# Kernel tuning notes

Hardware: AMD Instinct MI355X
Metric: run time of the kernel (lower is better)

The kernel has to match this reference:

```python
import jax, jax.numpy as jnp
import numpy as np

N, E = 50000, 1600000
FEAT, HID, HEADS = 256, 64, 2
NEG_SLOPE = 0.2


def gat_conv(x, src, dst, W, att_src, att_dst, bias, heads, out_ch):
    """PyG GATConv (concat=True, self-loops already appended to src/dst)."""
    n = x.shape[0]
    h = (x @ W).reshape(n, heads, out_ch)                      # [N,H,C]
    a_src = jnp.einsum('nhc,hc->nh', h, att_src)               # [N,H]
    a_dst = jnp.einsum('nhc,hc->nh', h, att_dst)               # [N,H]
    alpha = jax.nn.leaky_relu(a_src[src] + a_dst[dst], NEG_SLOPE)  # [E',H]
    # segment softmax over incoming edges of each dst node
    amax = jax.ops.segment_max(alpha, dst, num_segments=n)
    alpha = jnp.exp(alpha - amax[dst])
    denom = jax.ops.segment_sum(alpha, dst, num_segments=n)
    alpha = alpha / (denom[dst] + 1e-16)
    msg = h[src] * alpha[..., None]                            # [E',H,C]
    out = jax.ops.segment_sum(msg, dst, num_segments=n)        # [N,H,C]
    return out.reshape(n, heads * out_ch) + bias


def setup_inputs() -> dict:
    key = jax.random.key(0)
    ks = jax.random.split(key, 10)
    x = jax.random.normal(ks[0], (N, FEAT), dtype=jnp.float32)
    edge_index = jax.random.randint(ks[1], (2, E), 0, N, dtype=jnp.int64)
    s1 = 1.0 / np.sqrt(FEAT)
    s2 = 1.0 / np.sqrt(HID * HEADS)
    sa = 1.0 / np.sqrt(HID)
    return {
        'x': x,
        'edge_index': edge_index,
        'W1': jax.random.uniform(ks[2], (FEAT, HEADS * HID), jnp.float32, -s1, s1),
        'att_src1': jax.random.uniform(ks[3], (HEADS, HID), jnp.float32, -sa, sa),
        'att_dst1': jax.random.uniform(ks[4], (HEADS, HID), jnp.float32, -sa, sa),
        'b1': jnp.zeros((HEADS * HID,), jnp.float32),
        'W2': jax.random.uniform(ks[5], (HEADS * HID, HID), jnp.float32, -s2, s2),
        'att_src2': jax.random.uniform(ks[6], (1, HID), jnp.float32, -sa, sa),
        'att_dst2': jax.random.uniform(ks[7], (1, HID), jnp.float32, -sa, sa),
        'b2': jnp.zeros((HID,), jnp.float32),
    }


def reference(x, edge_index, W1, att_src1, att_dst1, b1, W2, att_src2, att_dst2, b2):
    n = x.shape[0]
    loop = jnp.arange(n, dtype=edge_index.dtype)
    src = jnp.concatenate([edge_index[0], loop])   # add self loops (PyG default)
    dst = jnp.concatenate([edge_index[1], loop])
    h = gat_conv(x, src, dst, W1, att_src1, att_dst1, b1, HEADS, HID)
    h = jax.nn.relu(h)  # dropout is identity in eval mode
    h = gat_conv(h, src, dst, W2, att_src2, att_dst2, b2, 1, HID)
    return jax.nn.log_softmax(h, axis=1)
```

## Files before the change

### kernel.cpp

```cpp
#include <hip/hip_runtime.h>
#include <hip/hip_bf16.h>
#include <math.h>

typedef short bf16x8 __attribute__((ext_vector_type(8)));
typedef float f32x4 __attribute__((ext_vector_type(4)));

#define BSHIFT 7
#define BWIDTH 128
#define PCHUNK 4096


__global__ void zero_buf(int* __restrict__ p, int n) {
    int i = blockIdx.x * blockDim.x + threadIdx.x;
    if (i < n) p[i] = 0;
}

__global__ __launch_bounds__(256) void bucket_hist(const int* __restrict__ ei, int E,
                                                   int* __restrict__ bcnt) {
    __shared__ int h[512];
    int tid = threadIdx.x;
    for (int i = tid; i < 512; i += 256) h[i] = 0;
    __syncthreads();
    int start = blockIdx.x * PCHUNK;
    int cnt = min(PCHUNK, E - start);
    for (int i = tid; i < cnt; i += 256)
        atomicAdd(&h[ei[E + start + i] >> BSHIFT], 1);
    __syncthreads();
    for (int i = tid; i < 512; i += 256)
        if (h[i]) atomicAdd(&bcnt[i], h[i]);
}

__global__ __launch_bounds__(512) void bucket_scan(const int* __restrict__ bcnt,
                                                   int* __restrict__ bbase,
                                                   int* __restrict__ bcur,
                                                   int nbk, int n) {
    __shared__ int s[512];
    int tid = threadIdx.x;
    int nodes = 0;
    if (tid < nbk) nodes = min(BWIDTH, n - (tid << BSHIFT));
    int v = (tid < nbk) ? bcnt[tid] + nodes : 0;
    s[tid] = v;
    __syncthreads();
    #pragma unroll
    for (int o = 1; o < 512; o <<= 1) {
        int t = (tid >= o) ? s[tid - o] : 0;
        __syncthreads();
        s[tid] += t;
        __syncthreads();
    }
    if (tid < nbk) {
        int ex = s[tid] - v;
        bbase[tid] = ex;
        bcur[tid] = ex - (tid << BSHIFT);
    }
    if (tid == nbk) bbase[nbk] = s[tid];
}

__global__ __launch_bounds__(256) void partition_edges(const int* __restrict__ ei, int E,
                                                       int* __restrict__ bcur,
                                                       int2* __restrict__ tmp) {
    __shared__ int2 stage[PCHUNK];
    __shared__ int h[512];
    __shared__ int lbase[512];
    int tid = threadIdx.x;
    int start = blockIdx.x * PCHUNK;
    int cnt = min(PCHUNK, E - start);
    for (int i = tid; i < 512; i += 256) h[i] = 0;
    __syncthreads();
    for (int i = tid; i < cnt; i += 256) {
        int s = ei[start + i];
        int d = ei[E + start + i];
        stage[i] = make_int2(s, d);
        atomicAdd(&h[d >> BSHIFT], 1);
    }
    __syncthreads();
    for (int i = tid; i < 512; i += 256) {
        if (h[i] > 0) lbase[i] = atomicAdd(&bcur[i], h[i]);
        h[i] = 0;
    }
    __syncthreads();
    for (int i = tid; i < cnt; i += 256) {
        int2 e = stage[i];
        int b = e.y >> BSHIFT;
        int r = atomicAdd(&h[b], 1);
        tmp[lbase[b] + r] = e;
    }
}

__global__ __launch_bounds__(256) void bucket_csr(const int* __restrict__ bbase,
                                                  const int2* __restrict__ tmp,
                                                  int* __restrict__ offs,
                                                  int* __restrict__ srcs,
                                                  int n, int nbk) {
    __shared__ int cnt[BWIDTH];
    __shared__ int sa[BWIDTH];
    __shared__ int cur[BWIDTH];
    int b = blockIdx.x;
    int tid = threadIdx.x;
    int node0 = b << BSHIFT;
    int nnodes = min(BWIDTH, n - node0);
    int cb = bbase[b];
    int ce = bbase[b + 1];
    int tb = cb - node0;
    int ecnt = (ce - cb) - nnodes;

    if (tid < BWIDTH) cnt[tid] = (tid < nnodes) ? 1 : 0;
    __syncthreads();
    for (int i = tid; i < ecnt; i += 256)
        atomicAdd(&cnt[tmp[tb + i].y & (BWIDTH - 1)], 1);
    __syncthreads();
    if (tid < BWIDTH) sa[tid] = cnt[tid];
    __syncthreads();
    #pragma unroll
    for (int o = 1; o < BWIDTH; o <<= 1) {
        int v = 0;
        if (tid < BWIDTH) { v = sa[tid]; if (tid >= o) v += sa[tid - o]; }
        __syncthreads();
        if (tid < BWIDTH) sa[tid] = v;
        __syncthreads();
    }
    if (tid < BWIDTH) {
        int ex = sa[tid] - cnt[tid];
        if (tid < nnodes) {
            offs[node0 + tid] = cb + ex;
            srcs[cb + ex] = node0 + tid;
        }
        cur[tid] = ex + (tid < nnodes ? 1 : 0);
    }
    if (b == nbk - 1 && tid == 0) offs[n] = ce;
    __syncthreads();
    for (int i = tid; i < ecnt; i += 256) {
        int2 e = tmp[tb + i];
        int li = e.y & (BWIDTH - 1);
        int r = atomicAdd(&cur[li], 1);
        srcs[cb + r] = e.x;
    }
}

__global__ void transpose_both(const float* __restrict__ W1, const float* __restrict__ W2,
                               __hip_bfloat16* __restrict__ W1t,
                               __hip_bfloat16* __restrict__ W2t) {
    int idx = blockIdx.x * blockDim.x + threadIdx.x;
    const int n1 = 128 * 256;
    if (idx < n1) {
        int nn = idx >> 8, kk = idx & 255;
        W1t[idx] = __float2bfloat16(W1[kk * 128 + nn]);
    } else {
        int j = idx - n1;
        if (j < 64 * 128) {
            int nn = j >> 7, kk = j & 127;
            W2t[j] = __float2bfloat16(W2[kk * 64 + nn]);
        }
    }
}

template <bool A_BF16, int NT, int HEADS>
__global__ __launch_bounds__(256) void gemm_att(
    const void* __restrict__ Av, const __hip_bfloat16* __restrict__ Bt,
    __hip_bfloat16* __restrict__ C,
    const float* __restrict__ atts, const float* __restrict__ attd,
    float* __restrict__ a_s, float* __restrict__ a_d, int M, int K) {
    constexpr int N = NT * 16;
    __shared__ __hip_bfloat16 As[64][40];
    int tid = threadIdx.x;
    int w = tid >> 6, l = tid & 63;
    int q = l >> 4, m16 = l & 15;
    int bm = blockIdx.x * 64;

    int lr = tid >> 2, lseg = tid & 3;
    int arow = bm + lr; if (arow >= M) arow = M - 1;

    f32x4 acc[NT];
    #pragma unroll
    for (int t = 0; t < NT; t++) acc[t] = (f32x4){0.f, 0.f, 0.f, 0.f};

    for (int kc = 0; kc < K; kc += 32) {
        if (A_BF16) {
            const __hip_bfloat16* A = (const __hip_bfloat16*)Av;
            uint4 v = *(const uint4*)(A + (size_t)arow * K + kc + lseg * 8);
            *(uint4*)&As[lr][lseg * 8] = v;
        } else {
            const float* A = (const float*)Av;
            float4 v0 = *(const float4*)(A + (size_t)arow * K + kc + lseg * 8);
            float4 v1 = *(const float4*)(A + (size_t)arow * K + kc + lseg * 8 + 4);
            union { __hip_bfloat16 h[8]; uint4 u; } tmp;
            tmp.h[0] = __float2bfloat16(v0.x); tmp.h[1] = __float2bfloat16(v0.y);
            tmp.h[2] = __float2bfloat16(v0.z); tmp.h[3] = __float2bfloat16(v0.w);
            tmp.h[4] = __float2bfloat16(v1.x); tmp.h[5] = __float2bfloat16(v1.y);
            tmp.h[6] = __float2bfloat16(v1.z); tmp.h[7] = __float2bfloat16(v1.w);
            *(uint4*)&As[lr][lseg * 8] = tmp.u;
        }
        __syncthreads();
        bf16x8 a = *(const bf16x8*)&As[w * 16 + m16][q * 8];
        #pragma unroll
        for (int t = 0; t < NT; t++) {
            bf16x8 b = *(const bf16x8*)(Bt + (size_t)(t * 16 + m16) * K + kc + q * 8);
            acc[t] = __builtin_amdgcn_mfma_f32_16x16x32_bf16(a, b, acc[t], 0, 0, 0);
        }
        __syncthreads();
    }

    #pragma unroll
    for (int t = 0; t < NT; t++) {
        #pragma unroll
        for (int r = 0; r < 4; r++) {
            int row = bm + w * 16 + q * 4 + r;
            if (row < M) C[(size_t)row * N + t * 16 + m16] = __float2bfloat16(acc[t][r]);
        }
    }

    float ps[HEADS][4], pd[HEADS][4];
    #pragma unroll
    for (int hh = 0; hh < HEADS; hh++)
        #pragma unroll
        for (int r = 0; r < 4; r++) { ps[hh][r] = 0.f; pd[hh][r] = 0.f; }
    #pragma unroll
    for (int t = 0; t < NT; t++) {
        int ch = t * 16 + m16;
        float asw = atts[ch], adw = attd[ch];
        int hh = (HEADS == 2) ? (t >> 2) : 0;
        #pragma unroll
        for (int r = 0; r < 4; r++) {
            ps[hh][r] = fmaf(acc[t][r], asw, ps[hh][r]);
            pd[hh][r] = fmaf(acc[t][r], adw, pd[hh][r]);
        }
    }
    #pragma unroll
    for (int o = 1; o < 16; o <<= 1) {
        #pragma unroll
        for (int hh = 0; hh < HEADS; hh++)
            #pragma unroll
            for (int r = 0; r < 4; r++) {
                ps[hh][r] += __shfl_xor(ps[hh][r], o);
                pd[hh][r] += __shfl_xor(pd[hh][r], o);
            }
    }
    if (m16 == 0) {
        #pragma unroll
        for (int r = 0; r < 4; r++) {
            int row = bm + w * 16 + q * 4 + r;
            if (row < M) {
                if (HEADS == 2) {
                    a_s[row * 2]     = ps[0][r];
                    a_s[row * 2 + 1] = ps[1][r];
                    a_d[row * 2]     = pd[0][r];
                    a_d[row * 2 + 1] = pd[1][r];
                } else {
                    a_s[row] = ps[0][r];
                    a_d[row] = pd[0][r];
                }
            }
        }
    }
}

__device__ __forceinline__ float leaky(float r) {
    return r < 0.f ? 0.2f * r : r;
}

__device__ __forceinline__ void unpack2(unsigned u, float& lo, float& hi) {
    lo = __uint_as_float(u << 16);
    hi = __uint_as_float(u & 0xffff0000u);
}

__global__ __launch_bounds__(256) void edge_agg_l1(
    const int* __restrict__ offs, const int* __restrict__ srcs,
    const __hip_bfloat16* __restrict__ h1, const float* __restrict__ asv,
    const float* __restrict__ adv, const float* __restrict__ bias,
    __hip_bfloat16* __restrict__ out, int n) {
    int d = (blockIdx.x * blockDim.x + threadIdx.x) >> 6;
    int lane = threadIdx.x & 63;
    if (d >= n) return;
    int start = offs[d], end = offs[d + 1];
    float ad0 = adv[2 * d], ad1 = adv[2 * d + 1];

    float m0 = -3.4e38f, m1 = -3.4e38f, s0 = 0.f, s1 = 0.f;
    for (int e = start + lane; e < end; e += 64) {
        int s = srcs[e];
        float2 a = *(const float2*)(asv + 2 * s);
        float r0 = leaky(a.x + ad0);
        float r1 = leaky(a.y + ad1);
        if (r0 > m0) { s0 *= __expf(m0 - r0); m0 = r0; }
        s0 += __expf(r0 - m0);
        if (r1 > m1) { s1 *= __expf(m1 - r1); m1 = r1; }
        s1 += __expf(r1 - m1);
    }
    #pragma unroll
    for (int o = 1; o < 64; o <<= 1) {
        float om0 = __shfl_xor(m0, o), os0 = __shfl_xor(s0, o);
        float nm0 = fmaxf(m0, om0);
        s0 = s0 * __expf(m0 - nm0) + os0 * __expf(om0 - nm0);
        m0 = nm0;
        float om1 = __shfl_xor(m1, o), os1 = __shfl_xor(s1, o);
        float nm1 = fmaxf(m1, om1);
        s1 = s1 * __expf(m1 - nm1) + os1 * __expf(om1 - nm1);
        m1 = nm1;
    }
    float inv0 = 1.f / (s0 + 1e-16f), inv1 = 1.f / (s1 + 1e-16f);

    int sub = lane & 15;
    int g = lane >> 4;
    int ch0 = sub * 8;
    int hsel = sub >> 3;

    float acc[8];
    #pragma unroll
    for (int k = 0; k < 8; k++) acc[k] = 0.f;

    for (int base = start; base < end; base += 64) {
        int cnt = min(64, end - base);
        int s_l = 0;
        float w0_l = 0.f, w1_l = 0.f;
        if (lane < cnt) {
            s_l = srcs[base + lane];
            float2 a = *(const float2*)(asv + 2 * s_l);
            w0_l = __expf(leaky(a.x + ad0) - m0) * inv0;
            w1_l = __expf(leaky(a.y + ad1) - m1) * inv1;
        }
        int steps = (cnt + 3) >> 2;
        for (int jj = 0; jj < steps; ++jj) {
            int e = jj * 4 + g;
            float w0e = __shfl(w0_l, e);
            float w1e = __shfl(w1_l, e);
            int se = __shfl(s_l, e);
            float we = hsel ? w1e : w0e;
            uint4 v = *(const uint4*)(h1 + (size_t)se * 128 + ch0);
            float f0, f1, f2, f3, f4, f5, f6, f7;
            unpack2(v.x, f0, f1);
            unpack2(v.y, f2, f3);
            unpack2(v.z, f4, f5);
            unpack2(v.w, f6, f7);
            acc[0] = fmaf(we, f0, acc[0]);
            acc[1] = fmaf(we, f1, acc[1]);
            acc[2] = fmaf(we, f2, acc[2]);
            acc[3] = fmaf(we, f3, acc[3]);
            acc[4] = fmaf(we, f4, acc[4]);
            acc[5] = fmaf(we, f5, acc[5]);
            acc[6] = fmaf(we, f6, acc[6]);
            acc[7] = fmaf(we, f7, acc[7]);
        }
    }
    #pragma unroll
    for (int o = 16; o < 64; o <<= 1)
        #pragma unroll
        for (int k = 0; k < 8; k++) acc[k] += __shfl_xor(acc[k], o);

    if (lane < 16) {
        float4 b0 = *(const float4*)(bias + ch0);
        float4 b1 = *(const float4*)(bias + ch0 + 4);
        union { __hip_bfloat16 h[8]; uint4 u; } o2;
        o2.h[0] = __float2bfloat16(fmaxf(acc[0] + b0.x, 0.f));
        o2.h[1] = __float2bfloat16(fmaxf(acc[1] + b0.y, 0.f));
        o2.h[2] = __float2bfloat16(fmaxf(acc[2] + b0.z, 0.f));
        o2.h[3] = __float2bfloat16(fmaxf(acc[3] + b0.w, 0.f));
        o2.h[4] = __float2bfloat16(fmaxf(acc[4] + b1.x, 0.f));
        o2.h[5] = __float2bfloat16(fmaxf(acc[5] + b1.y, 0.f));
        o2.h[6] = __float2bfloat16(fmaxf(acc[6] + b1.z, 0.f));
        o2.h[7] = __float2bfloat16(fmaxf(acc[7] + b1.w, 0.f));
        *(uint4*)(out + (size_t)d * 128 + ch0) = o2.u;
    }
}

__global__ __launch_bounds__(256) void edge_agg_l2(
    const int* __restrict__ offs, const int* __restrict__ srcs,
    const __hip_bfloat16* __restrict__ h2, const float* __restrict__ asv,
    const float* __restrict__ adv, const float* __restrict__ bias,
    float* __restrict__ out, int n) {
    int d = (blockIdx.x * blockDim.x + threadIdx.x) >> 6;
    int lane = threadIdx.x & 63;
    if (d >= n) return;
    int start = offs[d], end = offs[d + 1];
    float ad = adv[d];

    float m = -3.4e38f, ssum = 0.f;
    for (int e = start + lane; e < end; e += 64) {
        int s = srcs[e];
        float r = leaky(asv[s] + ad);
        if (r > m) { ssum *= __expf(m - r); m = r; }
        ssum += __expf(r - m);
    }
    #pragma unroll
    for (int o = 1; o < 64; o <<= 1) {
        float om = __shfl_xor(m, o), os = __shfl_xor(ssum, o);
        float nm = fmaxf(m, om);
        ssum = ssum * __expf(m - nm) + os * __expf(om - nm);
        m = nm;
    }
    float inv = 1.f / (ssum + 1e-16f);

    int sub = lane & 7;
    int g = lane >> 3;
    int ch0 = sub * 8;

    float acc[8];
    #pragma unroll
    for (int k = 0; k < 8; k++) acc[k] = 0.f;

    for (int base = start; base < end; base += 64) {
        int cnt = min(64, end - base);
        int s_l = 0;
        float w_l = 0.f;
        if (lane < cnt) {
            s_l = srcs[base + lane];
            w_l = __expf(leaky(asv[s_l] + ad) - m) * inv;
        }
        int steps = (cnt + 7) >> 3;
        for (int jj = 0; jj < steps; ++jj) {
            int e = jj * 8 + g;
            float we = __shfl(w_l, e);
            int se = __shfl(s_l, e);
            uint4 v = *(const uint4*)(h2 + (size_t)se * 64 + ch0);
            float f0, f1, f2, f3, f4, f5, f6, f7;
            unpack2(v.x, f0, f1);
            unpack2(v.y, f2, f3);
            unpack2(v.z, f4, f5);
            unpack2(v.w, f6, f7);
            acc[0] = fmaf(we, f0, acc[0]);
            acc[1] = fmaf(we, f1, acc[1]);
            acc[2] = fmaf(we, f2, acc[2]);
            acc[3] = fmaf(we, f3, acc[3]);
            acc[4] = fmaf(we, f4, acc[4]);
            acc[5] = fmaf(we, f5, acc[5]);
            acc[6] = fmaf(we, f6, acc[6]);
            acc[7] = fmaf(we, f7, acc[7]);
        }
    }
    #pragma unroll
    for (int o = 8; o < 64; o <<= 1)
        #pragma unroll
        for (int k = 0; k < 8; k++) acc[k] += __shfl_xor(acc[k], o);

    float4 b0 = *(const float4*)(bias + ch0);
    float4 b1 = *(const float4*)(bias + ch0 + 4);
    float v[8];
    v[0] = acc[0] + b0.x; v[1] = acc[1] + b0.y;
    v[2] = acc[2] + b0.z; v[3] = acc[3] + b0.w;
    v[4] = acc[4] + b1.x; v[5] = acc[5] + b1.y;
    v[6] = acc[6] + b1.z; v[7] = acc[7] + b1.w;

    float vm = v[0];
    #pragma unroll
    for (int k = 1; k < 8; k++) vm = fmaxf(vm, v[k]);
    #pragma unroll
    for (int o = 1; o < 8; o <<= 1) vm = fmaxf(vm, __shfl_xor(vm, o));
    float se_loc = 0.f;
    #pragma unroll
    for (int k = 0; k < 8; k++) se_loc += __expf(v[k] - vm);
    #pragma unroll
    for (int o = 1; o < 8; o <<= 1) se_loc += __shfl_xor(se_loc, o);
    float lse = vm + logf(se_loc);

    if (lane < 8) {
        float4 o0 = make_float4(v[0] - lse, v[1] - lse, v[2] - lse, v[3] - lse);
        float4 o1 = make_float4(v[4] - lse, v[5] - lse, v[6] - lse, v[7] - lse);
        *(float4*)(out + (size_t)d * 64 + ch0) = o0;
        *(float4*)(out + (size_t)d * 64 + ch0 + 4) = o1;
    }
}

extern "C" void kernel_launch(void* const* d_in, const int* in_sizes, int n_in,
                              void* d_out, int out_size, void* d_ws, size_t ws_size,
                              hipStream_t stream) {
    const float* x    = (const float*)d_in[0];
    const int*   ei   = (const int*)d_in[1];
    const float* W1   = (const float*)d_in[2];
    const float* as1w = (const float*)d_in[3];
    const float* ad1w = (const float*)d_in[4];
    const float* b1   = (const float*)d_in[5];
    const float* W2   = (const float*)d_in[6];
    const float* as2w = (const float*)d_in[7];
    const float* ad2w = (const float*)d_in[8];
    const float* b2   = (const float*)d_in[9];
    float* out = (float*)d_out;

    const int n = in_sizes[0] / 256;
    const int E = in_sizes[1] / 2;
    const int tot = E + n;
    const int nbk = (n + BWIDTH - 1) / BWIDTH;

    char* p = (char*)d_ws;
    auto alloc = [&](size_t bytes) {
        void* r = (void*)p;
        p += (bytes + 255) & ~(size_t)255;
        return r;
    };
    int*   offs  = (int*)alloc((size_t)(n + 1) * 4);
    int*   srcs  = (int*)alloc((size_t)tot * 4);
    int2*  tmp   = (int2*)alloc((size_t)E * 8);
    int*   bcnt  = (int*)alloc(512 * 4);
    int*   bbase = (int*)alloc(512 * 4);
    int*   bcur  = (int*)alloc(512 * 4);
    __hip_bfloat16* W1t = (__hip_bfloat16*)alloc((size_t)128 * 256 * 2);
    __hip_bfloat16* W2t = (__hip_bfloat16*)alloc((size_t)64 * 128 * 2);
    __hip_bfloat16* h1  = (__hip_bfloat16*)alloc((size_t)n * 128 * 2);
    __hip_bfloat16* out1= (__hip_bfloat16*)alloc((size_t)n * 128 * 2);
    __hip_bfloat16* h2  = (__hip_bfloat16*)alloc((size_t)n * 64 * 2);
    float* a_s1 = (float*)alloc((size_t)n * 2 * 4);
    float* a_d1 = (float*)alloc((size_t)n * 2 * 4);
    float* a_s2 = (float*)alloc((size_t)n * 4);
    float* a_d2 = (float*)alloc((size_t)n * 4);

    int pblocks = (E + PCHUNK - 1) / PCHUNK;

    zero_buf<<<2, 256, 0, stream>>>(bcnt, 512);
    bucket_hist<<<pblocks, 256, 0, stream>>>(ei, E, bcnt);
    bucket_scan<<<1, 512, 0, stream>>>(bcnt, bbase, bcur, nbk, n);
    partition_edges<<<pblocks, 256, 0, stream>>>(ei, E, bcur, tmp);
    bucket_csr<<<nbk, 256, 0, stream>>>(bbase, tmp, offs, srcs, n, nbk);

    transpose_both<<<(128 * 256 + 64 * 128 + 255) / 256, 256, 0, stream>>>(W1, W2, W1t, W2t);

    gemm_att<false, 8, 2><<<(n + 63) / 64, 256, 0, stream>>>(
        x, W1t, h1, as1w, ad1w, a_s1, a_d1, n, 256);
    edge_agg_l1<<<(n * 64 + 255) / 256, 256, 0, stream>>>(offs, srcs, h1, a_s1, a_d1, b1, out1, n);

    gemm_att<true, 4, 1><<<(n + 63) / 64, 256, 0, stream>>>(
        out1, W2t, h2, as2w, ad2w, a_s2, a_d2, n, 128);
    edge_agg_l2<<<(n * 64 + 255) / 256, 256, 0, stream>>>(offs, srcs, h2, a_s2, a_d2, b2, out, n);
}
```

Before: 306.1 us.

## Split layer-1 aggregation into one wavefront per head and pack partition temp entries

The layer-1 edge aggregation now assigns one 64-lane wavefront per (node, head) pair instead of per node. Each wavefront handles 64 channels with 8 edges in flight per step, which doubles the number of wavefronts and the concurrent gather parallelism. The cost is redundant reads of the CSR indices and source ids per head. Separately, the edge partition buffer packs src and local dst into a single int instead of an int2, halving that temp traffic; this relies on src << 7 fitting in 31 bits, which holds for n=50000.

New measurement: 319.4 us. +4.3%, slower.

```diff
diff --git a/kernel.cpp b/kernel.cpp
--- a/kernel.cpp
+++ b/kernel.cpp
@@ -58,7 +58,7 @@
 
 __global__ __launch_bounds__(256) void partition_edges(const int* __restrict__ ei, int E,
                                                        int* __restrict__ bcur,
-                                                       int2* __restrict__ tmp) {
+                                                       int* __restrict__ tmp) {
     __shared__ int2 stage[PCHUNK];
     __shared__ int h[512];
     __shared__ int lbase[512];
@@ -83,12 +83,12 @@
         int2 e = stage[i];
         int b = e.y >> BSHIFT;
         int r = atomicAdd(&h[b], 1);
-        tmp[lbase[b] + r] = e;
+        tmp[lbase[b] + r] = (e.x << BSHIFT) | (e.y & (BWIDTH - 1));
     }
 }
 
 __global__ __launch_bounds__(256) void bucket_csr(const int* __restrict__ bbase,
-                                                  const int2* __restrict__ tmp,
+                                                  const int* __restrict__ tmp,
                                                   int* __restrict__ offs,
                                                   int* __restrict__ srcs,
                                                   int n, int nbk) {
@@ -107,7 +107,7 @@
     if (tid < BWIDTH) cnt[tid] = (tid < nnodes) ? 1 : 0;
     __syncthreads();
     for (int i = tid; i < ecnt; i += 256)
-        atomicAdd(&cnt[tmp[tb + i].y & (BWIDTH - 1)], 1);
+        atomicAdd(&cnt[tmp[tb + i] & (BWIDTH - 1)], 1);
     __syncthreads();
     if (tid < BWIDTH) sa[tid] = cnt[tid];
     __syncthreads();
@@ -130,10 +130,10 @@
     if (b == nbk - 1 && tid == 0) offs[n] = ce;
     __syncthreads();
     for (int i = tid; i < ecnt; i += 256) {
-        int2 e = tmp[tb + i];
-        int li = e.y & (BWIDTH - 1);
+        int e = tmp[tb + i];
+        int li = e & (BWIDTH - 1);
         int r = atomicAdd(&cur[li], 1);
-        srcs[cb + r] = e.x;
+        srcs[cb + r] = e >> BSHIFT;
     }
 }
 
@@ -268,40 +268,33 @@
     const __hip_bfloat16* __restrict__ h1, const float* __restrict__ asv,
     const float* __restrict__ adv, const float* __restrict__ bias,
     __hip_bfloat16* __restrict__ out, int n) {
-    int d = (blockIdx.x * blockDim.x + threadIdx.x) >> 6;
+    int wid = (blockIdx.x * blockDim.x + threadIdx.x) >> 6;
     int lane = threadIdx.x & 63;
+    int d = wid >> 1;
+    int h = wid & 1;
     if (d >= n) return;
     int start = offs[d], end = offs[d + 1];
-    float ad0 = adv[2 * d], ad1 = adv[2 * d + 1];
-
-    float m0 = -3.4e38f, m1 = -3.4e38f, s0 = 0.f, s1 = 0.f;
+    float adh = adv[2 * d + h];
+
+    float m = -3.4e38f, ssum = 0.f;
     for (int e = start + lane; e < end; e += 64) {
         int s = srcs[e];
-        float2 a = *(const float2*)(asv + 2 * s);
-        float r0 = leaky(a.x + ad0);
-        float r1 = leaky(a.y + ad1);
-        if (r0 > m0) { s0 *= __expf(m0 - r0); m0 = r0; }
-        s0 += __expf(r0 - m0);
-        if (r1 > m1) { s1 *= __expf(m1 - r1); m1 = r1; }
-        s1 += __expf(r1 - m1);
+        float r = leaky(asv[2 * s + h] + adh);
+        if (r > m) { ssum *= __expf(m - r); m = r; }
+        ssum += __expf(r - m);
     }
     #pragma unroll
     for (int o = 1; o < 64; o <<= 1) {
-        float om0 = __shfl_xor(m0, o), os0 = __shfl_xor(s0, o);
-        float nm0 = fmaxf(m0, om0);
-        s0 = s0 * __expf(m0 - nm0) + os0 * __expf(om0 - nm0);
-        m0 = nm0;
-        float om1 = __shfl_xor(m1, o), os1 = __shfl_xor(s1, o);
-        float nm1 = fmaxf(m1, om1);
-        s1 = s1 * __expf(m1 - nm1) + os1 * __expf(om1 - nm1);
-        m1 = nm1;
-    }
-    float inv0 = 1.f / (s0 + 1e-16f), inv1 = 1.f / (s1 + 1e-16f);
-
-    int sub = lane & 15;
-    int g = lane >> 4;
-    int ch0 = sub * 8;
-    int hsel = sub >> 3;
+        float om = __shfl_xor(m, o), os = __shfl_xor(ssum, o);
+        float nm = fmaxf(m, om);
+        ssum = ssum * __expf(m - nm) + os * __expf(om - nm);
+        m = nm;
+    }
+    float inv = 1.f / (ssum + 1e-16f);
+
+    int sub = lane & 7;
+    int g = lane >> 3;
+    int ch0 = h * 64 + sub * 8;
 
     float acc[8];
     #pragma unroll
@@ -310,20 +303,16 @@
     for (int base = start; base < end; base += 64) {
         int cnt = min(64, end - base);
         int s_l = 0;
-        float w0_l = 0.f, w1_l = 0.f;
+        float w_l = 0.f;
         if (lane < cnt) {
             s_l = srcs[base + lane];
-            float2 a = *(const float2*)(asv + 2 * s_l);
-            w0_l = __expf(leaky(a.x + ad0) - m0) * inv0;
-            w1_l = __expf(leaky(a.y + ad1) - m1) * inv1;
-        }
-        int steps = (cnt + 3) >> 2;
+            w_l = __expf(leaky(asv[2 * s_l + h] + adh) - m) * inv;
+        }
+        int steps = (cnt + 7) >> 3;
         for (int jj = 0; jj < steps; ++jj) {
-            int e = jj * 4 + g;
-            float w0e = __shfl(w0_l, e);
-            float w1e = __shfl(w1_l, e);
+            int e = jj * 8 + g;
+            float we = __shfl(w_l, e);
             int se = __shfl(s_l, e);
-            float we = hsel ? w1e : w0e;
             uint4 v = *(const uint4*)(h1 + (size_t)se * 128 + ch0);
             float f0, f1, f2, f3, f4, f5, f6, f7;
             unpack2(v.x, f0, f1);
@@ -341,11 +330,11 @@
         }
     }
     #pragma unroll
-    for (int o = 16; o < 64; o <<= 1)
+    for (int o = 8; o < 64; o <<= 1)
         #pragma unroll
         for (int k = 0; k < 8; k++) acc[k] += __shfl_xor(acc[k], o);
 
-    if (lane < 16) {
+    if (lane < 8) {
         float4 b0 = *(const float4*)(bias + ch0);
         float4 b1 = *(const float4*)(bias + ch0 + 4);
         union { __hip_bfloat16 h[8]; uint4 u; } o2;
@@ -486,7 +475,7 @@
     };
     int*   offs  = (int*)alloc((size_t)(n + 1) * 4);
     int*   srcs  = (int*)alloc((size_t)tot * 4);
-    int2*  tmp   = (int2*)alloc((size_t)E * 8);
+    int*   tmp   = (int*)alloc((size_t)E * 4);
     int*   bcnt  = (int*)alloc(512 * 4);
     int*   bbase = (int*)alloc(512 * 4);
     int*   bcur  = (int*)alloc(512 * 4);
@@ -512,9 +501,11 @@
 
     gemm_att<false, 8, 2><<<(n + 63) / 64, 256, 0, stream>>>(
         x, W1t, h1, as1w, ad1w, a_s1, a_d1, n, 256);
-    edge_agg_l1<<<(n * 64 + 255) / 256, 256, 0, stream>>>(offs, srcs, h1, a_s1, a_d1, b1, out1, n);
+    edge_agg_l1<<<((size_t)n * 2 * 64 + 255) / 256, 256, 0, stream>>>(
+        offs, srcs, h1, a_s1, a_d1, b1, out1, n);
 
     gemm_att<true, 4, 1><<<(n + 63) / 64, 256, 0, stream>>>(
         out1, W2t, h2, as2w, ad2w, a_s2, a_d2, n, 128);
-    edge_agg_l2<<<(n * 64 + 255) / 256, 256, 0, stream>>>(offs, srcs, h2, a_s2, a_d2, b2, out, n);
-}
+    edge_agg_l2<<<((size_t)n * 64 + 255) / 256, 256, 0, stream>>>(
+        offs, srcs, h2, a_s2, a_d2, b2, out, n);
+}
```
